# Optimization experiments

Measured on AMD Instinct MI355X. Metric: run time of the kernel, lower is better.

Reference implementation:

```python
import jax, jax.numpy as jnp
import numpy as np

TEMPERATURE = 0.5
EPS = 1e-8  # torch F.cosine_similarity denominator clamp


def setup_inputs() -> dict:
    key = jax.random.key(0)
    k1, k2 = jax.random.split(key)
    B, D = 4096, 128
    return {
        "z_i": jax.random.normal(k1, (B, D), dtype=jnp.float32),
        "z_j": jax.random.normal(k2, (B, D), dtype=jnp.float32),
    }


def reference(z_i, z_j):
    B = z_i.shape[0]
    n2 = 2 * B
    reps = jnp.concatenate([z_i, z_j], axis=0)  # [2B, D]
    norms = jnp.maximum(jnp.linalg.norm(reps, axis=1, keepdims=True), EPS)
    rn = reps / norms
    # full pairwise cosine similarity matrix [2B, 2B]
    sim = rn @ rn.T
    # positives: sim[i, i+B] and sim[i+B, i]
    pos = jnp.concatenate([jnp.diagonal(sim, offset=B), jnp.diagonal(sim, offset=-B)])  # [2B]
    # Cross-entropy with label 0 on logits [pos, negatives]/T is equivalent to
    # -pos/T + logsumexp over {pos} U {negatives} = logsumexp over all j != i.
    diag_mask = jnp.eye(n2, dtype=bool)
    logits = jnp.where(diag_mask, -jnp.inf, sim / TEMPERATURE)
    lse = jax.nn.logsumexp(logits, axis=1)  # [2B]
    loss = jnp.sum(lse - pos / TEMPERATURE) / n2
    return loss
```

## Files before the change

### kernel.cpp

```cpp
#include <hip/hip_runtime.h>
#include <hip/hip_bf16.h>

#define B_ROWS 4096
#define N2     8192
#define DIM    128
#define LN2    0.6931471805599453f
#define S_SCALE 1.6986436f

typedef __attribute__((ext_vector_type(8))) short bf16x8;
typedef __attribute__((ext_vector_type(4))) float f32x4;

#if __has_builtin(__builtin_amdgcn_exp2f)
#define EXP2F(x) __builtin_amdgcn_exp2f(x)
#else
#define EXP2F(x) __expf((x) * LN2)
#endif
#if __has_builtin(__builtin_amdgcn_logf)
#define LOG2F_FAST(x) __builtin_amdgcn_logf(x)
#else
#define LOG2F_FAST(x) log2f(x)
#endif

static __device__ __forceinline__ unsigned short f2bf(float f) {
    union { float f; unsigned int u; } v; v.f = f;
    unsigned int u = v.u;
    return (unsigned short)((u + 0x7fffu + ((u >> 16) & 1u)) >> 16);
}
static __device__ __forceinline__ float bf2f(unsigned short s) {
    union { unsigned int u; float f; } v; v.u = ((unsigned int)s) << 16;
    return v.f;
}
static __device__ __forceinline__ void gload_lds16(const void* g, void* l) {
    __builtin_amdgcn_global_load_lds(
        (const __attribute__((address_space(1))) void*)g,
        (__attribute__((address_space(3))) void*)l, 16, 0, 0);
}

__global__ __launch_bounds__(256) void nk_normalize(
        const float* __restrict__ zi, const float* __restrict__ zj,
        unsigned short* __restrict__ rn, float* __restrict__ selfexp,
        float* __restrict__ out) {
    int gtid = blockIdx.x * 256 + threadIdx.x;
    if (gtid == 0) out[0] = 0.0f;
    int row  = gtid >> 6;
    int lane = threadIdx.x & 63;
    const float* src = (row < B_ROWS) ? (zi + (size_t)row * DIM)
                                      : (zj + (size_t)(row - B_ROWS) * DIM);
    float2 v = reinterpret_cast<const float2*>(src)[lane];
    float ss = v.x * v.x + v.y * v.y;
#pragma unroll
    for (int m = 1; m < 64; m <<= 1) ss += __shfl_xor(ss, m);
    float scale = S_SCALE / fmaxf(sqrtf(ss), 1e-8f);
    ushort2 o;
    o.x = f2bf(v.x * scale);
    o.y = f2bf(v.y * scale);
    reinterpret_cast<ushort2*>(rn + (size_t)row * DIM)[lane] = o;
    float a = bf2f(o.x), b = bf2f(o.y);
    float sd = a * a + b * b;
#pragma unroll
    for (int m = 1; m < 64; m <<= 1) sd += __shfl_xor(sd, m);
    if (lane == 0) selfexp[row] = EXP2F(sd);
}

__global__ __launch_bounds__(256, 4) void nk_simloss(
        const unsigned short* __restrict__ rn, float* __restrict__ part_out) {
    __shared__ char lds[2][16384];
    const int tid = threadIdx.x;
    const int bi = blockIdx.x >> 4;
    const int bc = blockIdx.x & 15;
    const int w = tid >> 6, lane = tid & 63;
    const int lc = lane & 15, lg = lane >> 4;
    const int i0 = bi * 128 + w * 32;

    const unsigned short* abase = rn + (size_t)(i0 + lc) * DIM + lg * 8;
    bf16x8 af[2][4];
#pragma unroll
    for (int mi = 0; mi < 2; ++mi)
#pragma unroll
        for (int ks = 0; ks < 4; ++ks)
            af[mi][ks] = *reinterpret_cast<const bf16x8*>(
                abase + (size_t)mi * 16 * DIM + ks * 32);

    const char* gsrc = (const char*)rn + (size_t)bc * 512 * 256;

#define STAGE(b, t)                                                           \
    do {                                                                      \
        _Pragma("unroll") for (int k = 0; k < 4; ++k) {                       \
            int L  = k * 4096 + tid * 16;                                     \
            int Ls = L ^ (((L >> 8) & 7) << 4);                               \
            gload_lds16(gsrc + (size_t)(t) * 16384 + Ls,                      \
                        &lds[b][k * 4096 + (tid & 192) * 16]);                \
        }                                                                     \
    } while (0)

    float part[2][4];
#pragma unroll
    for (int mi = 0; mi < 2; ++mi)
#pragma unroll
        for (int p = 0; p < 4; ++p) part[mi][p] = 0.f;

    STAGE(0, 0);

#pragma unroll 1
    for (int t = 0; t < 8; ++t) {
        const int cur = t & 1;
        __builtin_amdgcn_s_barrier();
        __builtin_amdgcn_sched_barrier(0);
        if (t < 7) {
            STAGE(cur ^ 1, t + 1);
            asm volatile("s_waitcnt vmcnt(4)" ::: "memory");
        } else {
            asm volatile("s_waitcnt vmcnt(0)" ::: "memory");
        }
        __builtin_amdgcn_s_barrier();
        __builtin_amdgcn_sched_barrier(0);
        const char* tb = lds[cur];
#pragma unroll
        for (int s = 0; s < 4; ++s) {
            bf16x8 bf[4];
#pragma unroll
            for (int ks = 0; ks < 4; ++ks) {
                int r = s * 16 + lc;
                int a = r * 256 + ks * 64 + lg * 16;
                a ^= (r & 7) << 4;
                bf[ks] = *reinterpret_cast<const bf16x8*>(tb + a);
            }
            f32x4 acc[2];
#pragma unroll
            for (int mi = 0; mi < 2; ++mi) acc[mi] = (f32x4){0.f, 0.f, 0.f, 0.f};
#pragma unroll
            for (int ks = 0; ks < 4; ++ks)
#pragma unroll
                for (int mi = 0; mi < 2; ++mi)
                    acc[mi] = __builtin_amdgcn_mfma_f32_16x16x32_bf16(
                        af[mi][ks], bf[ks], acc[mi], 0, 0, 0);
#pragma unroll
            for (int mi = 0; mi < 2; ++mi)
#pragma unroll
                for (int p = 0; p < 4; ++p)
                    part[mi][p] += EXP2F(acc[mi][p]);
        }
    }
#undef STAGE

#pragma unroll
    for (int mi = 0; mi < 2; ++mi)
#pragma unroll
        for (int p = 0; p < 4; ++p) {
            float v = part[mi][p];
#pragma unroll
            for (int m = 1; m < 16; m <<= 1) v += __shfl_xor(v, m);
            if (lc == 0)
                part_out[(size_t)bc * N2 + i0 + mi * 16 + lg * 4 + p] = v;
        }
}

__global__ __launch_bounds__(256) void nk_finalize(
        const unsigned short* __restrict__ rn, const float* __restrict__ part,
        const float* __restrict__ selfexp, float* __restrict__ out) {
    int wid = threadIdx.x >> 6, lane = threadIdx.x & 63;
    int lc = lane & 15, lg = lane >> 4;
    int wavegid = blockIdx.x * 4 + wid;
    float acc = 0.f;
    for (int base = wavegid * 4; base < N2; base += 512 * 4) {
        int row = base + lg;
        bf16x8 a = *reinterpret_cast<const bf16x8*>(rn + (size_t)row * DIM + lc * 8);
        bf16x8 b = *reinterpret_cast<const bf16x8*>(rn + (size_t)(row ^ B_ROWS) * DIM + lc * 8);
        float d = 0.f;
#pragma unroll
        for (int e = 0; e < 8; ++e)
            d += bf2f((unsigned short)a[e]) * bf2f((unsigned short)b[e]);
        float rs = part[(size_t)lc * N2 + row];
#pragma unroll
        for (int m = 1; m < 16; m <<= 1) {
            d  += __shfl_xor(d, m);
            rs += __shfl_xor(rs, m);
        }
        if (lc == 0)
            acc += LOG2F_FAST(rs - selfexp[row]) - d;
    }
#pragma unroll
    for (int m = 1; m < 64; m <<= 1) acc += __shfl_xor(acc, m);
    if (lane == 0) atomicAdd(out, acc * (LN2 / (float)N2));
}

extern "C" void kernel_launch(void* const* d_in, const int* in_sizes, int n_in,
                              void* d_out, int out_size, void* d_ws, size_t ws_size,
                              hipStream_t stream) {
    const float* zi = (const float*)d_in[0];
    const float* zj = (const float*)d_in[1];
    float* out = (float*)d_out;

    unsigned short* rn = (unsigned short*)d_ws;
    float* part    = (float*)((char*)d_ws + (size_t)N2 * DIM * 2);
    float* selfexp = part + 16 * N2;

    nk_normalize<<<2048, 256, 0, stream>>>(zi, zj, rn, selfexp, out);
    nk_simloss<<<1024, 256, 0, stream>>>(rn, part);
    nk_finalize<<<128, 256, 0, stream>>>(rn, part, selfexp, out);
}
```

Before: 90.90 us.

## Exploit similarity matrix symmetry by computing only upper-triangle tiles

Each block now computes a 128x128 tile of the similarity matrix chosen from a cyclic half-band, roughly half the 64x64 tile grid. Every tile's exp values feed both the row sums and, through column reductions with atomic adds, the transposed rows. The aim is to halve the MFMA and exp work of the dominant kernel. The price is many float atomics into a shared rowsum buffer, a changed per-block shape (2 tiles per block instead of 8), and a non-deterministic summation order.

```diff
diff --git a/kernel.cpp b/kernel.cpp
--- a/kernel.cpp
+++ b/kernel.cpp
@@ -39,8 +39,9 @@
 __global__ __launch_bounds__(256) void nk_normalize(
         const float* __restrict__ zi, const float* __restrict__ zj,
         unsigned short* __restrict__ rn, float* __restrict__ selfexp,
-        float* __restrict__ out) {
+        float* __restrict__ rowsum, float* __restrict__ out) {
     int gtid = blockIdx.x * 256 + threadIdx.x;
+    if (gtid < N2) rowsum[gtid] = 0.0f;
     if (gtid == 0) out[0] = 0.0f;
     int row  = gtid >> 6;
     int lane = threadIdx.x & 63;
@@ -63,14 +64,16 @@
 }
 
 __global__ __launch_bounds__(256, 4) void nk_simloss(
-        const unsigned short* __restrict__ rn, float* __restrict__ part_out) {
+        const unsigned short* __restrict__ rn, float* __restrict__ rowsum) {
     __shared__ char lds[2][16384];
     const int tid = threadIdx.x;
-    const int bi = blockIdx.x >> 4;
-    const int bc = blockIdx.x & 15;
+    const int a = blockIdx.x / 33;
+    const int b = blockIdx.x - a * 33;
+    if (b == 32 && a >= 32) return;
+    const int q = (a + b) & 63;
     const int w = tid >> 6, lane = tid & 63;
     const int lc = lane & 15, lg = lane >> 4;
-    const int i0 = bi * 128 + w * 32;
+    const int i0 = a * 128 + w * 32;
 
     const unsigned short* abase = rn + (size_t)(i0 + lc) * DIM + lg * 8;
     bf16x8 af[2][4];
@@ -81,15 +84,15 @@
             af[mi][ks] = *reinterpret_cast<const bf16x8*>(
                 abase + (size_t)mi * 16 * DIM + ks * 32);
 
-    const char* gsrc = (const char*)rn + (size_t)bc * 512 * 256;
-
-#define STAGE(b, t)                                                           \
+    const char* gsrc = (const char*)rn + (size_t)q * 128 * 256;
+
+#define STAGE(bbuf, t)                                                        \
     do {                                                                      \
         _Pragma("unroll") for (int k = 0; k < 4; ++k) {                       \
             int L  = k * 4096 + tid * 16;                                     \
             int Ls = L ^ (((L >> 8) & 7) << 4);                               \
             gload_lds16(gsrc + (size_t)(t) * 16384 + Ls,                      \
-                        &lds[b][k * 4096 + (tid & 192) * 16]);                \
+                        &lds[bbuf][k * 4096 + (tid & 192) * 16]);             \
         }                                                                     \
     } while (0)
 
@@ -102,11 +105,11 @@
     STAGE(0, 0);
 
 #pragma unroll 1
-    for (int t = 0; t < 8; ++t) {
+    for (int t = 0; t < 2; ++t) {
         const int cur = t & 1;
         __builtin_amdgcn_s_barrier();
         __builtin_amdgcn_sched_barrier(0);
-        if (t < 7) {
+        if (t < 1) {
             STAGE(cur ^ 1, t + 1);
             asm volatile("s_waitcnt vmcnt(4)" ::: "memory");
         } else {
@@ -115,15 +118,16 @@
         __builtin_amdgcn_s_barrier();
         __builtin_amdgcn_sched_barrier(0);
         const char* tb = lds[cur];
+        float colacc[4] = {0.f, 0.f, 0.f, 0.f};
 #pragma unroll
         for (int s = 0; s < 4; ++s) {
             bf16x8 bf[4];
 #pragma unroll
             for (int ks = 0; ks < 4; ++ks) {
                 int r = s * 16 + lc;
-                int a = r * 256 + ks * 64 + lg * 16;
-                a ^= (r & 7) << 4;
-                bf[ks] = *reinterpret_cast<const bf16x8*>(tb + a);
+                int ad = r * 256 + ks * 64 + lg * 16;
+                ad ^= (r & 7) << 4;
+                bf[ks] = *reinterpret_cast<const bf16x8*>(tb + ad);
             }
             f32x4 acc[2];
 #pragma unroll
@@ -137,8 +141,21 @@
 #pragma unroll
             for (int mi = 0; mi < 2; ++mi)
 #pragma unroll
-                for (int p = 0; p < 4; ++p)
-                    part[mi][p] += EXP2F(acc[mi][p]);
+                for (int p = 0; p < 4; ++p) {
+                    float e = EXP2F(acc[mi][p]);
+                    part[mi][p] += e;
+                    colacc[s]   += e;
+                }
+        }
+        if (b != 0) {
+#pragma unroll
+            for (int s = 0; s < 4; ++s) {
+                float cv = colacc[s];
+                cv += __shfl_xor(cv, 16);
+                cv += __shfl_xor(cv, 32);
+                if (lane < 16)
+                    atomicAdd(&rowsum[q * 128 + t * 64 + s * 16 + lc], cv);
+            }
         }
     }
 #undef STAGE
@@ -151,12 +168,12 @@
 #pragma unroll
             for (int m = 1; m < 16; m <<= 1) v += __shfl_xor(v, m);
             if (lc == 0)
-                part_out[(size_t)bc * N2 + i0 + mi * 16 + lg * 4 + p] = v;
+                atomicAdd(&rowsum[i0 + mi * 16 + lg * 4 + p], v);
         }
 }
 
 __global__ __launch_bounds__(256) void nk_finalize(
-        const unsigned short* __restrict__ rn, const float* __restrict__ part,
+        const unsigned short* __restrict__ rn, const float* __restrict__ rowsum,
         const float* __restrict__ selfexp, float* __restrict__ out) {
     int wid = threadIdx.x >> 6, lane = threadIdx.x & 63;
     int lc = lane & 15, lg = lane >> 4;
@@ -170,14 +187,10 @@
 #pragma unroll
         for (int e = 0; e < 8; ++e)
             d += bf2f((unsigned short)a[e]) * bf2f((unsigned short)b[e]);
-        float rs = part[(size_t)lc * N2 + row];
-#pragma unroll
-        for (int m = 1; m < 16; m <<= 1) {
-            d  += __shfl_xor(d, m);
-            rs += __shfl_xor(rs, m);
-        }
+#pragma unroll
+        for (int m = 1; m < 16; m <<= 1) d += __shfl_xor(d, m);
         if (lc == 0)
-            acc += LOG2F_FAST(rs - selfexp[row]) - d;
+            acc += LOG2F_FAST(rowsum[row] - selfexp[row]) - d;
     }
 #pragma unroll
     for (int m = 1; m < 64; m <<= 1) acc += __shfl_xor(acc, m);
@@ -192,10 +205,10 @@
     float* out = (float*)d_out;
 
     unsigned short* rn = (unsigned short*)d_ws;
-    float* part    = (float*)((char*)d_ws + (size_t)N2 * DIM * 2);
-    float* selfexp = part + 16 * N2;
-
-    nk_normalize<<<2048, 256, 0, stream>>>(zi, zj, rn, selfexp, out);
-    nk_simloss<<<1024, 256, 0, stream>>>(rn, part);
-    nk_finalize<<<128, 256, 0, stream>>>(rn, part, selfexp, out);
-}
+    float* rowsum  = (float*)((char*)d_ws + (size_t)N2 * DIM * 2);
+    float* selfexp = rowsum + N2;
+
+    nk_normalize<<<2048, 256, 0, stream>>>(zi, zj, rn, selfexp, rowsum, out);
+    nk_simloss<<<2112, 256, 0, stream>>>(rn, rowsum);
+    nk_finalize<<<128, 256, 0, stream>>>(rn, rowsum, selfexp, out);
+}
```

Measured after the change: 93.64 us. 1.03x slower.
